# Performance work log

Measured on AMD Instinct MI355X. Metric: run time of the kernel, lower is better.

## Reference

```python
import jax, jax.numpy as jnp
import numpy as np

NUM_USERS = 100_000
NUM_ITEMS = 50_000
N_TOTAL = 150_100
EMBED_DIM = 64
NUM_LAYERS = 3
N_EDGES = 3_000_000
BATCH = 4096


def setup_inputs() -> dict:
    key = jax.random.key(0)
    k1, k2, k3, k4, k5, k6 = jax.random.split(key, 6)
    node_emb = jax.random.normal(k1, (N_TOTAL, EMBED_DIM), dtype=jnp.float32) * 0.1
    # COO sparse normalized adjacency (static irregular pattern)
    adj_row = jax.random.randint(k2, (N_EDGES,), 0, N_TOTAL, dtype=jnp.int32)
    adj_col = jax.random.randint(k3, (N_EDGES,), 0, N_TOTAL, dtype=jnp.int32)
    adj_val = jax.random.uniform(k4, (N_EDGES,), dtype=jnp.float32) * 0.05
    user_ids = jax.random.randint(k5, (BATCH,), 0, NUM_USERS, dtype=jnp.int32)
    item_ids = jax.random.randint(k6, (BATCH,), 0, NUM_ITEMS, dtype=jnp.int32)
    return {"node_emb": node_emb, "adj_val": adj_val, "adj_row": adj_row,
            "adj_col": adj_col, "user_ids": user_ids, "item_ids": item_ids}


def reference(node_emb, adj_val, adj_row, adj_col, user_ids, item_ids):
    # LightGCN propagation: K sparse SpMM layers, running mean over K+1 embeddings
    emb = node_emb                       # [N, D] layer-0
    acc = emb                            # running sum instead of stack+mean
    for _ in range(NUM_LAYERS):
        # SpMM: out[r] += val * emb[c]   (COO scatter-add)
        msgs = adj_val[:, None] * emb[adj_col]          # [E, D]
        emb = jax.ops.segment_sum(msgs, adj_row, num_segments=N_TOTAL)
        acc = acc + emb
    final = acc / jnp.float32(NUM_LAYERS + 1)           # mean over layers
    users = final[:NUM_USERS]
    items = final[NUM_USERS:NUM_USERS + NUM_ITEMS]
    u = users[user_ids]                                 # [B, D]
    i = items[item_ids]                                 # [B, D]
    return (u * i).sum(axis=-1)                         # [B]
```

## Files before the change

### kernel.cpp

```cpp
#include <hip/hip_runtime.h>

#define N_TOTAL    150100
#define NUM_USERS  100000
#define DIM        64
#define BSHIFT     8
#define BROWS      (1 << BSHIFT)
#define NBUK       ((N_TOTAL + BROWS - 1) / BROWS)
#define EPB        4096
#define EPT        16
#define CAP        5632
#define RSP        260

#define VSCALE     262144.0f
#define VINV       (1.0f / 262144.0f)

__device__ __forceinline__ int wave_incl_scan(int x, int lane) {
    #pragma unroll
    for (int off = 1; off < 64; off <<= 1) {
        int y = __shfl_up(x, off, 64);
        if (lane >= off) x += y;
    }
    return x;
}

__device__ __forceinline__ float ub0(unsigned w) { return (float)(w & 0xFFu); }
__device__ __forceinline__ float ub1(unsigned w) { return (float)((w >> 8) & 0xFFu); }
__device__ __forceinline__ float ub2(unsigned w) { return (float)((w >> 16) & 0xFFu); }
__device__ __forceinline__ float ub3(unsigned w) { return (float)(w >> 24); }

__device__ __forceinline__ unsigned quant_pack(float4 f, float inv) {
    int a = __float2int_rn(f.x * inv) + 128;
    int b = __float2int_rn(f.y * inv) + 128;
    int c = __float2int_rn(f.z * inv) + 128;
    int d = __float2int_rn(f.w * inv) + 128;
    a = min(max(a, 0), 255); b = min(max(b, 0), 255);
    c = min(max(c, 0), 255); d = min(max(d, 0), 255);
    return (unsigned)a | ((unsigned)b << 8) | ((unsigned)c << 16) | ((unsigned)d << 24);
}

__global__ void convert_quant(const float4* __restrict__ in4,
                              unsigned* __restrict__ q, float* __restrict__ sc,
                              int* __restrict__ gcount) {
    int t = blockIdx.x * blockDim.x + threadIdx.x;
    if (t < NBUK) gcount[t] = 0;
    int r = t >> 4, sl = t & 15;
    if (r >= N_TOTAL) return;
    float4 f = in4[(size_t)r * 16 + sl];
    float m = fmaxf(fmaxf(fabsf(f.x), fabsf(f.y)), fmaxf(fabsf(f.z), fabsf(f.w)));
    #pragma unroll
    for (int off = 1; off < 16; off <<= 1) m = fmaxf(m, __shfl_xor(m, off, 64));
    float inv = (m > 1e-30f) ? 127.0f / m : 0.0f;
    q[(size_t)r * 16 + sl] = quant_pack(f, inv);
    if (sl == 0) sc[r] = m * (1.0f / 127.0f);
}

__global__ void __launch_bounds__(256, 4) fill_buckets(
        const int* __restrict__ rows, const int* __restrict__ cols,
        const float* __restrict__ vals, int n_edges,
        int* __restrict__ gcount,
        uint2* __restrict__ epk8) {
    __shared__ unsigned      payb[EPB];
    __shared__ unsigned char rowb[EPB];
    __shared__ short         tgtb[EPB];
    __shared__ int hist[NBUK];
    __shared__ int pref[NBUK];
    __shared__ int cur[NBUK];
    __shared__ int loc[NBUK];
    __shared__ int wtot[4];
    const int tid = threadIdx.x;
    const int lane = tid & 63, wid = tid >> 6;
    const int base = blockIdx.x * EPB;
    int end = base + EPB; if (end > n_edges) end = n_edges;
    const int cnt = end - base;

    for (int i = tid; i < NBUK; i += 256) hist[i] = 0;

    unsigned pay[EPT];
    unsigned er[EPT];
    __syncthreads();

    if (cnt == EPB) {
        #pragma unroll
        for (int g = 0; g < 4; ++g) {
            const int e = base + (g * 256 + tid) * 4;
            int4   r4 = *(const int4*)(rows + e);
            int4   c4 = *(const int4*)(cols + e);
            float4 v4 = *(const float4*)(vals + e);
            int rr[4] = { r4.x, r4.y, r4.z, r4.w };
            int cc[4] = { c4.x, c4.y, c4.z, c4.w };
            float vv[4] = { v4.x, v4.y, v4.z, v4.w };
            #pragma unroll
            for (int k = 0; k < 4; ++k) {
                const int j = g * 4 + k;
                int q = (int)(vv[k] * VSCALE + 0.5f);
                if (q > 16383) q = 16383;
                pay[j] = ((unsigned)cc[k] << 14) | (unsigned)q;
                er[j]  = (unsigned)rr[k];
                atomicAdd(&hist[rr[k] >> BSHIFT], 1);
            }
        }
    } else {
        #pragma unroll
        for (int g = 0; g < 4; ++g) {
            const int e0 = base + (g * 256 + tid) * 4;
            #pragma unroll
            for (int k = 0; k < 4; ++k) {
                const int j = g * 4 + k;
                const int e = e0 + k;
                if (e < end) {
                    int r = rows[e];
                    int q = (int)(vals[e] * VSCALE + 0.5f);
                    if (q > 16383) q = 16383;
                    pay[j] = ((unsigned)cols[e] << 14) | (unsigned)q;
                    er[j]  = (unsigned)r;
                    atomicAdd(&hist[r >> BSHIFT], 1);
                } else {
                    er[j] = 0xFFFFFFFFu;
                }
            }
        }
    }
    __syncthreads();

    for (int b = tid; b < NBUK; b += 256) {
        int h = hist[b];
        loc[b] = h ? atomicAdd(&gcount[b], h) : 0;
    }
    const int t0 = tid * 3;
    int t1 = t0 + 3; if (t1 > NBUK) t1 = NBUK;
    int s = 0;
    for (int i = t0; i < t1; ++i) s += hist[i];
    int incl = wave_incl_scan(s, lane);
    if (lane == 63) wtot[wid] = incl;
    __syncthreads();
    int wofs = 0;
    for (int w = 0; w < wid; ++w) wofs += wtot[w];
    int run = incl + wofs - s;
    for (int i = t0; i < t1; ++i) {
        int h = hist[i];
        pref[i] = run;
        cur[i] = run;
        run += h;
    }
    __syncthreads();

    #pragma unroll
    for (int j = 0; j < EPT; ++j) {
        unsigned r = er[j];
        if (r != 0xFFFFFFFFu) {
            int b = (int)(r >> BSHIFT);
            int pos = atomicAdd(&cur[b], 1);
            payb[pos] = pay[j];
            rowb[pos] = (unsigned char)(r & (BROWS - 1));
            tgtb[pos] = (short)b;
        }
    }
    __syncthreads();

    for (int i = tid; i < cnt; i += 256) {
        int b = tgtb[i];
        int o = loc[b] + (i - pref[b]);
        if (o < CAP) {
            epk8[(size_t)b * CAP + o] = make_uint2(payb[i], (unsigned)rowb[i]);
        }
    }
}

__global__ void __launch_bounds__(256) bucket_sort(
        uint2* __restrict__ epk8,
        const int* __restrict__ gcount,
        int* __restrict__ rs) {
    __shared__ unsigned      buf[CAP];
    __shared__ unsigned char rbuf[CAP];
    __shared__ int hist[BROWS];
    __shared__ int curl[BROWS];
    __shared__ int wtot[4];
    const int tid = threadIdx.x;
    const int lane = tid & 63, wid = tid >> 6;
    const int b = blockIdx.x;
    const size_t k0 = (size_t)b * CAP;
    int cnt = gcount[b]; if (cnt > CAP) cnt = CAP;

    hist[tid] = 0;
    __syncthreads();
    for (int i = tid; i < cnt; i += 256) {
        uint2 e = epk8[k0 + i];
        buf[i]  = e.x;
        rbuf[i] = (unsigned char)e.y;
        atomicAdd(&hist[e.y & 255u], 1);
    }
    __syncthreads();
    int s = hist[tid];
    int incl = wave_incl_scan(s, lane);
    if (lane == 63) wtot[wid] = incl;
    __syncthreads();
    int wofs = 0;
    for (int w = 0; w < wid; ++w) wofs += wtot[w];
    int ex = incl + wofs - s;
    const int rbase = b << BSHIFT;
    int nrow = N_TOTAL - rbase; if (nrow > BROWS) nrow = BROWS;
    const int o0 = 2 * b * CAP;
    if (tid < nrow) rs[b * RSP + tid] = o0 + ex;
    if (tid == 0) rs[b * RSP + nrow] = o0 + cnt;
    curl[tid] = ex;
    __syncthreads();
    unsigned* out = (unsigned*)epk8;
    for (int i = tid; i < cnt; i += 256) {
        int rl = rbuf[i];
        int pos = atomicAdd(&curl[rl], 1);
        out[o0 + pos] = buf[i];
    }
}


#define SPMM_EDGE(J)                                                          \
    {                                                                         \
        unsigned e = (unsigned)__shfl((int)pr, subbase + (J), 64);            \
        int c = (int)(e >> 14);                                               \
        uint4 w = *(const uint4*)(qt + (size_t)c * 16 + (sl << 2));           \
        float vs = (float)(e & 16383u) * VINV * sc[c];                        \
        corr += vs;                                                           \
        sA.x += vs * ub0(w.x); sA.y += vs * ub1(w.x);                         \
        sA.z += vs * ub2(w.x); sA.w += vs * ub3(w.x);                         \
        sB.x += vs * ub0(w.y); sB.y += vs * ub1(w.y);                         \
        sB.z += vs * ub2(w.y); sB.w += vs * ub3(w.y);                         \
        sC.x += vs * ub0(w.z); sC.y += vs * ub1(w.z);                         \
        sC.z += vs * ub2(w.z); sC.w += vs * ub3(w.z);                         \
        sD.x += vs * ub0(w.w); sD.y += vs * ub1(w.w);                         \
        sD.z += vs * ub2(w.w); sD.w += vs * ub3(w.w);                         \
    }

__global__ void spmm_q8(const unsigned* __restrict__ qt,
                        const float* __restrict__ sc,
                        const int* __restrict__ rs,
                        const unsigned* __restrict__ epk,
                        unsigned* __restrict__ qo,
                        float* __restrict__ so) {
    int t = blockIdx.x * blockDim.x + threadIdx.x;
    int r = t >> 2;
    int sl = t & 3;
    int lane = threadIdx.x & 63;
    int subbase = lane & 60;
    if (r >= N_TOTAL) return;
    const int* rsb = rs + (r >> BSHIFT) * RSP + (r & (BROWS - 1));
    int k0 = rsb[0], k1 = rsb[1];
    float4 sA = make_float4(0.f, 0.f, 0.f, 0.f);
    float4 sB = make_float4(0.f, 0.f, 0.f, 0.f);
    float4 sC = make_float4(0.f, 0.f, 0.f, 0.f);
    float4 sD = make_float4(0.f, 0.f, 0.f, 0.f);
    float corr = 0.f;
    for (int kb = k0; kb < k1; kb += 4) {
        int cnt = k1 - kb; if (cnt > 4) cnt = 4;
        unsigned pr = (sl < cnt) ? epk[kb + sl] : 0u;
        if (cnt == 4) {
            SPMM_EDGE(0) SPMM_EDGE(1) SPMM_EDGE(2) SPMM_EDGE(3)
        } else {
            for (int j = 0; j < cnt; ++j) SPMM_EDGE(j)
        }
    }
    float c128 = 128.0f * corr;
    sA.x -= c128; sA.y -= c128; sA.z -= c128; sA.w -= c128;
    sB.x -= c128; sB.y -= c128; sB.z -= c128; sB.w -= c128;
    sC.x -= c128; sC.y -= c128; sC.z -= c128; sC.w -= c128;
    sD.x -= c128; sD.y -= c128; sD.z -= c128; sD.w -= c128;
    float mA = fmaxf(fmaxf(fabsf(sA.x), fabsf(sA.y)), fmaxf(fabsf(sA.z), fabsf(sA.w)));
    float mB = fmaxf(fmaxf(fabsf(sB.x), fabsf(sB.y)), fmaxf(fabsf(sB.z), fabsf(sB.w)));
    float mC = fmaxf(fmaxf(fabsf(sC.x), fabsf(sC.y)), fmaxf(fabsf(sC.z), fabsf(sC.w)));
    float mD = fmaxf(fmaxf(fabsf(sD.x), fabsf(sD.y)), fmaxf(fabsf(sD.z), fabsf(sD.w)));
    float m = fmaxf(fmaxf(mA, mB), fmaxf(mC, mD));
    m = fmaxf(m, __shfl_xor(m, 1, 64));
    m = fmaxf(m, __shfl_xor(m, 2, 64));
    float inv = (m > 1e-30f) ? 127.0f / m : 0.0f;
    uint4 o = make_uint4(quant_pack(sA, inv), quant_pack(sB, inv),
                         quant_pack(sC, inv), quant_pack(sD, inv));
    *(uint4*)(qo + (size_t)r * 16 + (sl << 2)) = o;
    if (sl == 0) so[r] = m * (1.0f / 127.0f);
}

__device__ __forceinline__ float4 dec4(unsigned w, float s) {
    return make_float4(s * (ub0(w) - 128.0f), s * (ub1(w) - 128.0f),
                       s * (ub2(w) - 128.0f), s * (ub3(w) - 128.0f));
}

__device__ __forceinline__ float4 rowsum_q8(const unsigned* __restrict__ qt,
                                            const float* __restrict__ sc,
                                            const int* __restrict__ rs,
                                            const unsigned* __restrict__ epk,
                                            int r, int sl, int subbase) {
    const int* rsb = rs + (r >> BSHIFT) * RSP + (r & (BROWS - 1));
    int k0 = rsb[0], k1 = rsb[1];
    float4 s = make_float4(0.f, 0.f, 0.f, 0.f);
    float corr = 0.f;
    for (int kb = k0; kb < k1; kb += 16) {
        int cnt = k1 - kb; if (cnt > 16) cnt = 16;
        unsigned pr = (sl < cnt) ? epk[kb + sl] : 0u;
        for (int j = 0; j < cnt; ++j) {
            unsigned e = (unsigned)__shfl((int)pr, subbase + j, 64);
            int c = e >> 14;
            unsigned w = qt[(size_t)c * 16 + sl];
            float vs = (float)(e & 16383u) * VINV * sc[c];
            corr += vs;
            s.x += vs * ub0(w); s.y += vs * ub1(w);
            s.z += vs * ub2(w); s.w += vs * ub3(w);
        }
    }
    float c128 = 128.0f * corr;
    s.x -= c128; s.y -= c128; s.z -= c128; s.w -= c128;
    return s;
}

__global__ void final_dot_fused(const float4* __restrict__ emb4,
                                const unsigned* __restrict__ q1,
                                const float* __restrict__ s1,
                                const unsigned* __restrict__ q2,
                                const float* __restrict__ s2,
                                const int* __restrict__ rs,
                                const unsigned* __restrict__ epk,
                                const int* __restrict__ user_ids,
                                const int* __restrict__ item_ids,
                                float* __restrict__ out, int batch) {
    int t = blockIdx.x * blockDim.x + threadIdx.x;
    int b = t >> 4, sl = t & 15;
    int lane = threadIdx.x & 63;
    int subbase = lane & 48;
    if (b >= batch) return;
    int u = user_ids[b];
    int iN = NUM_USERS + item_ids[b];

    float4 lu = rowsum_q8(q2, s2, rs, epk, u, sl, subbase);
    float4 li = rowsum_q8(q2, s2, rs, epk, iN, sl, subbase);

    float4 nu = emb4[(size_t)u * 16 + sl];
    float4 au = dec4(q1[(size_t)u * 16 + sl], s1[u]);
    float4 bu = dec4(q2[(size_t)u * 16 + sl], s2[u]);
    float4 ni = emb4[(size_t)iN * 16 + sl];
    float4 ai = dec4(q1[(size_t)iN * 16 + sl], s1[iN]);
    float4 bi = dec4(q2[(size_t)iN * 16 + sl], s2[iN]);

    float ux = nu.x + au.x + bu.x + lu.x;
    float uy = nu.y + au.y + bu.y + lu.y;
    float uz = nu.z + au.z + bu.z + lu.z;
    float uw = nu.w + au.w + bu.w + lu.w;
    float ix = ni.x + ai.x + bi.x + li.x;
    float iy = ni.y + ai.y + bi.y + li.y;
    float iz = ni.z + ai.z + bi.z + li.z;
    float iw = ni.w + ai.w + bi.w + li.w;

    float s = ux * ix + uy * iy + uz * iz + uw * iw;
    #pragma unroll
    for (int off = 8; off > 0; off >>= 1) s += __shfl_down(s, off, 64);
    if (sl == 0) out[b] = s * (1.0f / 16.0f);
}


static inline size_t align256(size_t x) { return (x + 255) & ~(size_t)255; }

extern "C" void kernel_launch(void* const* d_in, const int* in_sizes, int n_in,
                              void* d_out, int out_size, void* d_ws, size_t ws_size,
                              hipStream_t stream) {
    const float* node_emb = (const float*)d_in[0];
    const float* adj_val  = (const float*)d_in[1];
    const int*   adj_row  = (const int*)d_in[2];
    const int*   adj_col  = (const int*)d_in[3];
    const int*   user_ids = (const int*)d_in[4];
    const int*   item_ids = (const int*)d_in[5];
    float* out = (float*)d_out;

    const int n_edges = in_sizes[1];
    const int batch   = in_sizes[4];

    const size_t qtab_bytes = (size_t)N_TOTAL * 16 * sizeof(unsigned);
    const size_t sc_bytes   = (size_t)N_TOTAL * sizeof(float);

    char* p = (char*)d_ws;
    size_t off = 0;
    unsigned* q0 = (unsigned*)(p + off); off = align256(off + qtab_bytes);
    unsigned* q1 = (unsigned*)(p + off); off = align256(off + qtab_bytes);
    unsigned* q2 = (unsigned*)(p + off); off = align256(off + qtab_bytes);
    float* s0    = (float*)(p + off);    off = align256(off + sc_bytes);
    float* s1    = (float*)(p + off);    off = align256(off + sc_bytes);
    float* s2    = (float*)(p + off);    off = align256(off + sc_bytes);
    int* gcount  = (int*)(p + off);      off = align256(off + (size_t)NBUK * sizeof(int));
    int* rs      = (int*)(p + off);      off = align256(off + (size_t)NBUK * RSP * sizeof(int));
    uint2* epk8  = (uint2*)(p + off);    off = align256(off + (size_t)NBUK * CAP * sizeof(uint2));
    (void)ws_size;

    const int nbf = (n_edges + EPB - 1) / EPB;
    const int rblocks = ((N_TOTAL * 16) + 255) / 256;
    const int sblocks = ((N_TOTAL * 4) + 255) / 256;

    convert_quant<<<rblocks, 256, 0, stream>>>(
        (const float4*)node_emb, q0, s0, gcount);

    fill_buckets<<<nbf, 256, 0, stream>>>(adj_row, adj_col, adj_val, n_edges,
                                          gcount, epk8);
    bucket_sort<<<NBUK, 256, 0, stream>>>(epk8, gcount, rs);

    const unsigned* epk = (const unsigned*)epk8;

    spmm_q8<<<sblocks, 256, 0, stream>>>(q0, s0, rs, epk, q1, s1);
    spmm_q8<<<sblocks, 256, 0, stream>>>(q1, s1, rs, epk, q2, s2);

    {
        int threads = batch * 16;
        final_dot_fused<<<(threads + 255) / 256, 256, 0, stream>>>(
            (const float4*)node_emb, q1, s1, q2, s2, rs, epk,
            user_ids, item_ids, out, batch);
    }
}
```

Measured before the change: 300.3 us.

## Use eight lanes per row in quantized SpMM and precompute edge scales per lane

```diff
diff --git a/kernel.cpp b/kernel.cpp
--- a/kernel.cpp
+++ b/kernel.cpp
@@ -213,23 +213,6 @@
 }
 
 
-#define SPMM_EDGE(J)                                                          \
-    {                                                                         \
-        unsigned e = (unsigned)__shfl((int)pr, subbase + (J), 64);            \
-        int c = (int)(e >> 14);                                               \
-        uint4 w = *(const uint4*)(qt + (size_t)c * 16 + (sl << 2));           \
-        float vs = (float)(e & 16383u) * VINV * sc[c];                        \
-        corr += vs;                                                           \
-        sA.x += vs * ub0(w.x); sA.y += vs * ub1(w.x);                         \
-        sA.z += vs * ub2(w.x); sA.w += vs * ub3(w.x);                         \
-        sB.x += vs * ub0(w.y); sB.y += vs * ub1(w.y);                         \
-        sB.z += vs * ub2(w.y); sB.w += vs * ub3(w.y);                         \
-        sC.x += vs * ub0(w.z); sC.y += vs * ub1(w.z);                         \
-        sC.z += vs * ub2(w.z); sC.w += vs * ub3(w.z);                         \
-        sD.x += vs * ub0(w.w); sD.y += vs * ub1(w.w);                         \
-        sD.z += vs * ub2(w.w); sD.w += vs * ub3(w.w);                         \
-    }
-
 __global__ void spmm_q8(const unsigned* __restrict__ qt,
                         const float* __restrict__ sc,
                         const int* __restrict__ rs,
@@ -237,43 +220,49 @@
                         unsigned* __restrict__ qo,
                         float* __restrict__ so) {
     int t = blockIdx.x * blockDim.x + threadIdx.x;
-    int r = t >> 2;
-    int sl = t & 3;
+    int r = t >> 3;
+    int sl = t & 7;
     int lane = threadIdx.x & 63;
-    int subbase = lane & 60;
+    int subbase = lane & 56;
     if (r >= N_TOTAL) return;
     const int* rsb = rs + (r >> BSHIFT) * RSP + (r & (BROWS - 1));
     int k0 = rsb[0], k1 = rsb[1];
     float4 sA = make_float4(0.f, 0.f, 0.f, 0.f);
     float4 sB = make_float4(0.f, 0.f, 0.f, 0.f);
-    float4 sC = make_float4(0.f, 0.f, 0.f, 0.f);
-    float4 sD = make_float4(0.f, 0.f, 0.f, 0.f);
     float corr = 0.f;
-    for (int kb = k0; kb < k1; kb += 4) {
-        int cnt = k1 - kb; if (cnt > 4) cnt = 4;
-        unsigned pr = (sl < cnt) ? epk[kb + sl] : 0u;
-        if (cnt == 4) {
-            SPMM_EDGE(0) SPMM_EDGE(1) SPMM_EDGE(2) SPMM_EDGE(3)
-        } else {
-            for (int j = 0; j < cnt; ++j) SPMM_EDGE(j)
-        }
-    }
+    const unsigned* qrow = qt + (sl << 1);
+    for (int kb = k0; kb < k1; kb += 8) {
+        unsigned pr = epk[kb + sl];
+        if (sl >= k1 - kb) pr = 0u;
+        float vsl = (float)(pr & 16383u) * VINV * sc[pr >> 14];
+        corr += vsl;
+        #pragma unroll
+        for (int j = 0; j < 8; ++j) {
+            unsigned e = (unsigned)__shfl((int)pr, subbase + j, 64);
+            float vs = __shfl(vsl, subbase + j, 64);
+            int c = (int)(e >> 14);
+            uint2 w = *(const uint2*)(qrow + ((size_t)c << 4));
+            sA.x += vs * ub0(w.x); sA.y += vs * ub1(w.x);
+            sA.z += vs * ub2(w.x); sA.w += vs * ub3(w.x);
+            sB.x += vs * ub0(w.y); sB.y += vs * ub1(w.y);
+            sB.z += vs * ub2(w.y); sB.w += vs * ub3(w.y);
+        }
+    }
+    corr += __shfl_xor(corr, 1, 64);
+    corr += __shfl_xor(corr, 2, 64);
+    corr += __shfl_xor(corr, 4, 64);
     float c128 = 128.0f * corr;
     sA.x -= c128; sA.y -= c128; sA.z -= c128; sA.w -= c128;
     sB.x -= c128; sB.y -= c128; sB.z -= c128; sB.w -= c128;
-    sC.x -= c128; sC.y -= c128; sC.z -= c128; sC.w -= c128;
-    sD.x -= c128; sD.y -= c128; sD.z -= c128; sD.w -= c128;
     float mA = fmaxf(fmaxf(fabsf(sA.x), fabsf(sA.y)), fmaxf(fabsf(sA.z), fabsf(sA.w)));
     float mB = fmaxf(fmaxf(fabsf(sB.x), fabsf(sB.y)), fmaxf(fabsf(sB.z), fabsf(sB.w)));
-    float mC = fmaxf(fmaxf(fabsf(sC.x), fabsf(sC.y)), fmaxf(fabsf(sC.z), fabsf(sC.w)));
-    float mD = fmaxf(fmaxf(fabsf(sD.x), fabsf(sD.y)), fmaxf(fabsf(sD.z), fabsf(sD.w)));
-    float m = fmaxf(fmaxf(mA, mB), fmaxf(mC, mD));
+    float m = fmaxf(mA, mB);
     m = fmaxf(m, __shfl_xor(m, 1, 64));
     m = fmaxf(m, __shfl_xor(m, 2, 64));
+    m = fmaxf(m, __shfl_xor(m, 4, 64));
     float inv = (m > 1e-30f) ? 127.0f / m : 0.0f;
-    uint4 o = make_uint4(quant_pack(sA, inv), quant_pack(sB, inv),
-                         quant_pack(sC, inv), quant_pack(sD, inv));
-    *(uint4*)(qo + (size_t)r * 16 + (sl << 2)) = o;
+    uint2 o = make_uint2(quant_pack(sA, inv), quant_pack(sB, inv));
+    *(uint2*)(qo + (size_t)r * 16 + (sl << 1)) = o;
     if (sl == 0) so[r] = m * (1.0f / 127.0f);
 }
 
@@ -387,7 +376,7 @@
 
     const int nbf = (n_edges + EPB - 1) / EPB;
     const int rblocks = ((N_TOTAL * 16) + 255) / 256;
-    const int sblocks = ((N_TOTAL * 4) + 255) / 256;
+    const int sblocks = ((N_TOTAL * 8) + 255) / 256;
 
     convert_quant<<<rblocks, 256, 0, stream>>>(
         (const float4*)node_emb, q0, s0, gcount);
```

Result: faster. 278.2 us (-7.4%).
